# Performance work log

Hardware: AMD Instinct MI355X
Metric: run time of the kernel (lower is better)

Reference implementation:

```python
import jax, jax.numpy as jnp
import numpy as np

D_MODEL = 1024
N_HEADS = 16
HEAD_DIM = D_MODEL // N_HEADS


def setup_inputs() -> dict:
    key = jax.random.key(0)
    ks = jax.random.split(key, 12)
    B, L = 2, 2048
    s = 1.0 / np.sqrt(D_MODEL)
    inp = {
        "q": jax.random.normal(ks[0], (B, L, D_MODEL), dtype=jnp.float32),
        "k": jax.random.normal(ks[1], (B, L, D_MODEL), dtype=jnp.float32),
        "v": jax.random.normal(ks[2], (B, L, D_MODEL), dtype=jnp.float32),
        "mask": jax.random.randint(ks[3], (B, L), 0, 2).astype(jnp.bool_),
        "Wq": jax.random.normal(ks[4], (D_MODEL, D_MODEL), dtype=jnp.float32) * s,
        "bq": jnp.zeros((D_MODEL,), dtype=jnp.float32),
        "Wk": jax.random.normal(ks[5], (D_MODEL, D_MODEL), dtype=jnp.float32) * s,
        "bk": jnp.zeros((D_MODEL,), dtype=jnp.float32),
        "Wv": jax.random.normal(ks[6], (D_MODEL, D_MODEL), dtype=jnp.float32) * s,
        "bv": jnp.zeros((D_MODEL,), dtype=jnp.float32),
        "Wo": jax.random.normal(ks[7], (D_MODEL, D_MODEL), dtype=jnp.float32) * s,
        "bo": jnp.zeros((D_MODEL,), dtype=jnp.float32),
    }
    return inp


def reference(q, k, v, mask, Wq, bq, Wk, bk, Wv, bv, Wo, bo):
    B, Lq, _ = q.shape
    Lk = k.shape[1]
    # torch Linear: y = x @ W.T + b; W is [out, in]
    Q = (jnp.einsum("bld,ed->ble", q, Wq) + bq).reshape(B, Lq, N_HEADS, HEAD_DIM).transpose(0, 2, 1, 3)
    K = (jnp.einsum("bld,ed->ble", k, Wk) + bk).reshape(B, Lk, N_HEADS, HEAD_DIM).transpose(0, 2, 1, 3)
    V = (jnp.einsum("bld,ed->ble", v, Wv) + bv).reshape(B, Lk, N_HEADS, HEAD_DIM).transpose(0, 2, 1, 3)
    scale = 1.0 / np.sqrt(HEAD_DIM).astype(np.float32)
    scores = jnp.einsum("bhqd,bhkd->bhqk", Q, K) * scale  # [B,H,Lq,Lk]
    # mask: True = masked out; broadcast (B,1,1,Lk)
    scores = jnp.where(mask[:, None, None, :], -jnp.inf, scores)
    attn = jax.nn.softmax(scores, axis=-1)
    out = jnp.einsum("bhqk,bhkd->bhqd", attn, V)  # [B,H,Lq,hd]
    out = out.transpose(0, 2, 1, 3).reshape(B, Lq, D_MODEL)
    return jnp.einsum("bld,ed->ble", out, Wo) + bo
```

## Files before the change

kernel.cpp:

```cpp
#include <hip/hip_runtime.h>

typedef unsigned short u16;
typedef __bf16 bf16x8 __attribute__((ext_vector_type(8)));
typedef float f32x4 __attribute__((ext_vector_type(4)));
typedef unsigned int u32x4 __attribute__((ext_vector_type(4)));
typedef unsigned int u32x2 __attribute__((ext_vector_type(2)));

#define MFMA16(a, b, c) __builtin_amdgcn_mfma_f32_16x16x32_bf16((a), (b), (c), 0, 0, 0)

__device__ __forceinline__ u16 f2bf(float f) {
    unsigned u = __builtin_bit_cast(unsigned, f);
    u = u + 0x7FFFu + ((u >> 16) & 1u);
    return (u16)(u >> 16);
}
__device__ __forceinline__ unsigned pk2(float a, float b) {
    return (unsigned)f2bf(a) | ((unsigned)f2bf(b) << 16);
}
__device__ __forceinline__ u32x4 pk8(f32x4 a, f32x4 b) {
    u32x4 r;
    r[0] = pk2(a[0], a[1]); r[1] = pk2(a[2], a[3]);
    r[2] = pk2(b[0], b[1]); r[3] = pk2(b[2], b[3]);
    return r;
}
__device__ __forceinline__ unsigned cvtpk(float a, float b) {
    unsigned r;
    asm("v_cvt_pk_bf16_f32 %0, %1, %2" : "=v"(r) : "v"(a), "v"(b));
    return r;
}
__device__ __forceinline__ float exp2_fast(float x) {
    float r;
    asm("v_exp_f32 %0, %1" : "=v"(r) : "v"(x));
    return r;
}
__device__ __forceinline__ void lds_load16(const u16* g, u16* l) {
    __builtin_amdgcn_global_load_lds(
        (const __attribute__((address_space(1))) void*)g,
        (__attribute__((address_space(3))) void*)l, 16, 0, 0);
}

#define QSCALE 0.18033688011112042f
#define FIXMAX 13.0f

__global__ __launch_bounds__(256) void convert_bf16(
    const float* __restrict__ q, const float* __restrict__ k, const float* __restrict__ v,
    const float* __restrict__ Wq, const float* __restrict__ Wk, const float* __restrict__ Wv,
    const float* __restrict__ Wo, u16* __restrict__ dst)
{
    const size_t i = ((size_t)blockIdx.x * 256 + threadIdx.x) * 8;
    const size_t QE = 4194304, WE = 1048576;
    const float* s;
    if (i < QE) s = q + i;
    else if (i < 2 * QE) s = k + (i - QE);
    else if (i < 3 * QE) s = v + (i - 2 * QE);
    else {
        size_t j = i - 3 * QE;
        if (j < WE) s = Wq + j;
        else if (j < 2 * WE) s = Wk + (j - WE);
        else if (j < 3 * WE) s = Wv + (j - 2 * WE);
        else s = Wo + (j - 3 * WE);
    }
    f32x4 a = *(const f32x4*)s;
    f32x4 b = *(const f32x4*)(s + 4);
    *(u32x4*)(dst + i) = pk8(a, b);
}

template <bool SW>
__device__ __forceinline__ void gemm128_core(
    const u16* __restrict__ A, const u16* __restrict__ B,
    int m0, int n0, u16* As, u16* Bs, int tid, f32x4 acc[4][4])
{
    const int wv = tid >> 6, lane = tid & 63, quad = lane >> 4, l16 = lane & 15;
    const int mh = (wv >> 1) * 64, nh = (wv & 1) * 64;
    const int segA0 = wv * 128 + lane;
    const int segA1 = wv * 128 + 64 + lane;
    const int ra0 = segA0 >> 2, ca0 = (segA0 & 3) * 8;
    const int ra1 = segA1 >> 2, ca1 = (segA1 & 3) * 8;
    u16* ldsA0 = &As[(wv * 128) * 8];
    u16* ldsA1 = &As[(wv * 128 + 64) * 8];
    u16* ldsB0 = &Bs[(wv * 128) * 8];
    u16* ldsB1 = &Bs[(wv * 128 + 64) * 8];
    const u16* gA = A + (size_t)m0 * 1024;
    const u16* gB = B + (size_t)n0 * 1024;

    for (int t = 0; t < 32; t++) {
        const int k0 = t * 32;
        __syncthreads();
        lds_load16(gA + (size_t)ra0 * 1024 + k0 + ca0, ldsA0);
        lds_load16(gA + (size_t)ra1 * 1024 + k0 + ca1, ldsA1);
        lds_load16(gB + (size_t)ra0 * 1024 + k0 + ca0, ldsB0);
        lds_load16(gB + (size_t)ra1 * 1024 + k0 + ca1, ldsB1);
        __syncthreads();
        bf16x8 af[4], bfr[4];
        #pragma unroll
        for (int mi = 0; mi < 4; mi++)
            af[mi] = *(const bf16x8*)&As[(mh + mi * 16 + l16) * 32 + quad * 8];
        #pragma unroll
        for (int ni = 0; ni < 4; ni++)
            bfr[ni] = *(const bf16x8*)&Bs[(nh + ni * 16 + l16) * 32 + quad * 8];
        #pragma unroll
        for (int mi = 0; mi < 4; mi++)
            #pragma unroll
            for (int ni = 0; ni < 4; ni++)
                acc[mi][ni] = SW ? MFMA16(bfr[ni], af[mi], acc[mi][ni])
                                 : MFMA16(af[mi], bfr[ni], acc[mi][ni]);
    }
}

__global__ __launch_bounds__(256) void qkv_bf(
    const u16* __restrict__ qb, const u16* __restrict__ kb, const u16* __restrict__ vb,
    const u16* __restrict__ wq, const u16* __restrict__ wk, const u16* __restrict__ wvv,
    const float* __restrict__ bq, const float* __restrict__ bk, const float* __restrict__ bv,
    u16* __restrict__ Qh, u16* __restrict__ Kh, u16* __restrict__ Vt)
{
    __shared__ alignas(16) u16 As[128 * 32];
    __shared__ alignas(16) u16 Bs[128 * 32];
    const int z = blockIdx.z;
    const u16* A = (z == 0) ? qb : (z == 1) ? kb : vb;
    const u16* B = (z == 0) ? wq : (z == 1) ? wk : wvv;
    const float* bias = (z == 0) ? bq : (z == 1) ? bk : bv;
    const int tid = threadIdx.x;
    const int id = blockIdx.x + (blockIdx.y << 3);
    const int xd = id >> 5;
    const int yd = ((id & 7) << 2) | ((id >> 3) & 3);
    const int m0 = yd * 128, n0 = xd * 128;
    const int wv = tid >> 6, lane = tid & 63, quad = lane >> 4, l16 = lane & 15;
    const int mh = (wv >> 1) * 64, nh = (wv & 1) * 64;

    f32x4 acc[4][4];
    #pragma unroll
    for (int i = 0; i < 4; i++)
        #pragma unroll
        for (int j = 0; j < 4; j++) acc[i][j] = (f32x4){0.f, 0.f, 0.f, 0.f};

    if (z == 2) gemm128_core<true>(A, B, m0, n0, As, Bs, tid, acc);
    else        gemm128_core<false>(A, B, m0, n0, As, Bs, tid, acc);

    if (z < 2) {
        const float scl = (z == 0) ? QSCALE : 1.0f;
        u16* outp = (z == 0) ? Qh : Kh;
        #pragma unroll
        for (int ni = 0; ni < 4; ni++) {
            const int n = n0 + nh + ni * 16 + l16;
            const float bval = bias[n];
            const int h = n >> 6, d = n & 63;
            #pragma unroll
            for (int mi = 0; mi < 4; mi++) {
                const int mbase = m0 + mh + mi * 16 + quad * 4;
                #pragma unroll
                for (int r = 0; r < 4; r++) {
                    const int m = mbase + r;
                    const int bb = m >> 11, l = m & 2047;
                    const float val = (acc[mi][ni][r] + bval) * scl;
                    outp[(((size_t)(bb * 16 + h) * 2048 + l) << 6) + d] = f2bf(val);
                }
            }
        }
    } else {
        const int mW = m0 + mh;
        const int bb = mW >> 11;
        const int l0 = mW & 2047;
        #pragma unroll
        for (int ni = 0; ni < 4; ni++) {
            const int nb = n0 + nh + ni * 16 + quad * 4;
            const f32x4 bv4 = *(const f32x4*)&bias[nb];
            const int h = nb >> 6, d0 = nb & 63;
            u16* vrow = Vt + ((size_t)(bb * 16 + h) * 64 + d0) * 2048;
            #pragma unroll
            for (int mi = 0; mi < 4; mi++) {
                const int l = l0 + mi * 16 + l16;
                #pragma unroll
                for (int r = 0; r < 4; r++)
                    vrow[(size_t)r * 2048 + l] = f2bf(acc[mi][ni][r] + bv4[r]);
            }
        }
    }
}

__global__ __launch_bounds__(256) void out_bf(
    const u16* __restrict__ Ob, const u16* __restrict__ wo,
    const float* __restrict__ bo, float* __restrict__ out)
{
    __shared__ alignas(16) u16 As[128 * 32];
    __shared__ alignas(16) u16 Bs[128 * 32];
    const int tid = threadIdx.x;
    const int id = blockIdx.x + (blockIdx.y << 3);
    const int xd = id >> 5;
    const int yd = ((id & 7) << 2) | ((id >> 3) & 3);
    const int m0 = yd * 128, n0 = xd * 128;
    const int wv = tid >> 6, lane = tid & 63, quad = lane >> 4, l16 = lane & 15;
    const int mh = (wv >> 1) * 64, nh = (wv & 1) * 64;

    f32x4 acc[4][4];
    #pragma unroll
    for (int i = 0; i < 4; i++)
        #pragma unroll
        for (int j = 0; j < 4; j++) acc[i][j] = (f32x4){0.f, 0.f, 0.f, 0.f};

    gemm128_core<false>(Ob, wo, m0, n0, As, Bs, tid, acc);

    #pragma unroll
    for (int ni = 0; ni < 4; ni++) {
        const int n = n0 + nh + ni * 16 + l16;
        const float bval = bo[n];
        #pragma unroll
        for (int mi = 0; mi < 4; mi++) {
            const int mbase = m0 + mh + mi * 16 + quad * 4;
            #pragma unroll
            for (int r = 0; r < 4; r++)
                out[(size_t)(mbase + r) * 1024 + n] = acc[mi][ni][r] + bval;
        }
    }
}

__global__ __launch_bounds__(256) void attn10(
    const u16* __restrict__ Qh, const u16* __restrict__ Kh,
    const u16* __restrict__ Vt, const int* __restrict__ mask,
    u16* __restrict__ Ob)
{
    __shared__ alignas(16) u16 Ks[2][64 * 64];
    __shared__ alignas(16) u16 Vs[2][64 * 64];
    __shared__ alignas(16) float Ms[2][64];

    const int tid = threadIdx.x;
    const int blk = blockIdx.x;
    const int bh = blk & 31, qt = blk >> 5;
    const int b = bh >> 4, h = bh & 15;
    const int wv = tid >> 6, lane = tid & 63, quad = lane >> 4, l16 = lane & 15;

    const int qbase = qt * 128 + wv * 32;
    const u16* Qb = Qh + ((size_t)bh * 2048 + qbase) * 64;
    bf16x8 qf[2][2];
    #pragma unroll
    for (int sub = 0; sub < 2; sub++)
        #pragma unroll
        for (int hf = 0; hf < 2; hf++)
            qf[sub][hf] = *(const bf16x8*)(Qb + (sub * 16 + l16) * 64 + hf * 32 + quad * 8);

    const u32x4 onebits = {0x3F803F80u, 0x3F803F80u, 0x3F803F80u, 0x3F803F80u};
    const bf16x8 onesf = __builtin_bit_cast(bf16x8, onebits);

    const u16* Kb = Kh + (size_t)bh * 2048 * 64;
    const u16* Vb = Vt + (size_t)bh * 64 * 2048;
    const int* mb = mask + b * 2048;

    const int urow = lane >> 3;
    const int cunit = (lane & 7) ^ urow;
    const int u0 = wv * 16 + urow, u1 = u0 + 8;
    const int ki0 = (u0 & 3) | (((u0 >> 4) & 1) << 2) | (((u0 >> 2) & 3) << 3) | ((u0 >> 5) << 5);
    const int ki1 = (u1 & 3) | (((u1 >> 4) & 1) << 2) | (((u1 >> 2) & 3) << 3) | ((u1 >> 5) << 5);
    const u16* gk0 = Kb + (size_t)ki0 * 64 + cunit * 8;
    const u16* gk1 = Kb + (size_t)ki1 * 64 + cunit * 8;
    const u16* gv0 = Vb + (size_t)u0 * 2048 + cunit * 8;
    const u16* gv1 = Vb + (size_t)u1 * 2048 + cunit * 8;

    lds_load16(gk0, &Ks[0][wv * 1024]);
    lds_load16(gk1, &Ks[0][wv * 1024 + 512]);
    lds_load16(gv0, &Vs[0][wv * 1024]);
    lds_load16(gv1, &Vs[0][wv * 1024 + 512]);
    float rm = (tid < 64) ? (mb[tid] ? -1e30f : -FIXMAX) : 0.f;

    f32x4 o[2][4];
    #pragma unroll
    for (int sub = 0; sub < 2; sub++)
        #pragma unroll
        for (int db = 0; db < 4; db++) o[sub][db] = (f32x4){0.f, 0.f, 0.f, 0.f};
    f32x4 accL[2];
    accL[0] = (f32x4){0.f, 0.f, 0.f, 0.f};
    accL[1] = (f32x4){0.f, 0.f, 0.f, 0.f};

    const int x0 = l16 & 7;

    for (int kc = 0; kc < 32; kc++) {
        const int bi = kc & 1;
        if (tid < 64) Ms[bi][tid] = rm;
        __syncthreads();

        if (kc < 31) {
            const int off = (kc + 1) * 64;
            const int nbi = bi ^ 1;
            lds_load16(gk0 + (size_t)off * 64, &Ks[nbi][wv * 1024]);
            lds_load16(gk1 + (size_t)off * 64, &Ks[nbi][wv * 1024 + 512]);
            lds_load16(gv0 + off, &Vs[nbi][wv * 1024]);
            lds_load16(gv1 + off, &Vs[nbi][wv * 1024 + 512]);
            rm = (tid < 64) ? (mb[off + tid] ? -1e30f : -FIXMAX) : 0.f;
        }

        const u16* KsB = Ks[bi];
        const u16* VsB = Vs[bi];

        f32x4 st[2][4];
        __builtin_amdgcn_s_setprio(1);
        #pragma unroll
        for (int nb = 0; nb < 4; nb++) {
            const f32x4 mneg = *(const f32x4*)&Ms[bi][((nb >> 1) << 5) + (quad << 3) + ((nb & 1) << 2)];
            const bf16x8 kf0 = *(const bf16x8*)&KsB[(nb * 16 + l16) * 64 + ((quad ^ x0) << 3)];
            const bf16x8 kf1 = *(const bf16x8*)&KsB[(nb * 16 + l16) * 64 + (((4 | quad) ^ x0) << 3)];
            #pragma unroll
            for (int sub = 0; sub < 2; sub++) {
                f32x4 z = mneg;
                z = MFMA16(kf0, qf[sub][0], z);
                z = MFMA16(kf1, qf[sub][1], z);
                st[sub][nb] = z;
            }
        }
        __builtin_amdgcn_s_setprio(0);

        bf16x8 pf[2][2];
        #pragma unroll
        for (int sub = 0; sub < 2; sub++) {
            #pragma unroll
            for (int nb = 0; nb < 4; nb++)
                #pragma unroll
                for (int r = 0; r < 4; r++) st[sub][nb][r] = exp2_fast(st[sub][nb][r]);
            u32x4 w0, w1;
            w0[0] = cvtpk(st[sub][0][0], st[sub][0][1]);
            w0[1] = cvtpk(st[sub][0][2], st[sub][0][3]);
            w0[2] = cvtpk(st[sub][1][0], st[sub][1][1]);
            w0[3] = cvtpk(st[sub][1][2], st[sub][1][3]);
            w1[0] = cvtpk(st[sub][2][0], st[sub][2][1]);
            w1[1] = cvtpk(st[sub][2][2], st[sub][2][3]);
            w1[2] = cvtpk(st[sub][3][0], st[sub][3][1]);
            w1[3] = cvtpk(st[sub][3][2], st[sub][3][3]);
            pf[sub][0] = __builtin_bit_cast(bf16x8, w0);
            pf[sub][1] = __builtin_bit_cast(bf16x8, w1);
        }

        __builtin_amdgcn_s_setprio(1);
        #pragma unroll
        for (int db = 0; db < 4; db++) {
            const bf16x8 vf0 = *(const bf16x8*)&VsB[(db * 16 + l16) * 64 + ((quad ^ x0) << 3)];
            const bf16x8 vf1 = *(const bf16x8*)&VsB[(db * 16 + l16) * 64 + (((4 | quad) ^ x0) << 3)];
            #pragma unroll
            for (int sub = 0; sub < 2; sub++) {
                o[sub][db] = MFMA16(pf[sub][0], vf0, o[sub][db]);
                o[sub][db] = MFMA16(pf[sub][1], vf1, o[sub][db]);
            }
        }
        #pragma unroll
        for (int sub = 0; sub < 2; sub++) {
            accL[sub] = MFMA16(pf[sub][0], onesf, accL[sub]);
            accL[sub] = MFMA16(pf[sub][1], onesf, accL[sub]);
        }
        __builtin_amdgcn_s_setprio(0);
        asm volatile("" ::: "memory");
    }

    #pragma unroll
    for (int sub = 0; sub < 2; sub++) {
        #pragma unroll
        for (int r = 0; r < 4; r++) {
            const float lr = __builtin_amdgcn_rcpf(accL[sub][r]);
            const int qrow = qt * 128 + wv * 32 + sub * 16 + quad * 4 + r;
            #pragma unroll
            for (int db = 0; db < 4; db++)
                Ob[((size_t)(b * 2048 + qrow)) * 1024 + h * 64 + db * 16 + l16] =
                    f2bf(o[sub][db][r] * lr);
        }
    }
}

__global__ __launch_bounds__(256) void qkv_gemm(
    const float* __restrict__ q, const float* __restrict__ k, const float* __restrict__ v,
    const float* __restrict__ Wq, const float* __restrict__ Wk, const float* __restrict__ Wv,
    const float* __restrict__ bq, const float* __restrict__ bk, const float* __restrict__ bv,
    u16* __restrict__ Qh, u16* __restrict__ Kh, u16* __restrict__ Vt)
{
    __shared__ alignas(16) u16 As[128 * 40];
    __shared__ alignas(16) u16 Bs[128 * 40];
    const int z = blockIdx.z;
    const float* A    = (z == 0) ? q  : (z == 1) ? k  : v;
    const float* W    = (z == 0) ? Wq : (z == 1) ? Wk : Wv;
    const float* bias = (z == 0) ? bq : (z == 1) ? bk : bv;
    const int tid = threadIdx.x;
    const int m0 = blockIdx.y * 128, n0 = blockIdx.x * 128;
    const int row = tid >> 1, cseg = tid & 1;
    const float* ga = A + (size_t)(m0 + row) * 1024 + cseg * 16;
    const float* gb = W + (size_t)(n0 + row) * 1024 + cseg * 16;
    const int wv = tid >> 6, lane = tid & 63, quad = lane >> 4, l16 = lane & 15;
    const int mh = (wv >> 1) * 64, nh = (wv & 1) * 64;

    f32x4 acc[4][4];
    for (int i = 0; i < 4; i++)
        for (int j = 0; j < 4; j++) acc[i][j] = (f32x4){0.f, 0.f, 0.f, 0.f};

    f32x4 ra[4], rb[4];
    for (int i = 0; i < 4; i++) {
        ra[i] = *(const f32x4*)(ga + i * 4);
        rb[i] = *(const f32x4*)(gb + i * 4);
    }
    for (int t = 0; t < 32; t++) {
        __syncthreads();
        *(u32x4*)&As[row * 40 + cseg * 16]     = pk8(ra[0], ra[1]);
        *(u32x4*)&As[row * 40 + cseg * 16 + 8] = pk8(ra[2], ra[3]);
        *(u32x4*)&Bs[row * 40 + cseg * 16]     = pk8(rb[0], rb[1]);
        *(u32x4*)&Bs[row * 40 + cseg * 16 + 8] = pk8(rb[2], rb[3]);
        __syncthreads();
        if (t < 31) {
            const int k0 = (t + 1) * 32;
            for (int i = 0; i < 4; i++) {
                ra[i] = *(const f32x4*)(ga + k0 + i * 4);
                rb[i] = *(const f32x4*)(gb + k0 + i * 4);
            }
        }
        bf16x8 af[4], bfr[4];
        for (int mi = 0; mi < 4; mi++)
            af[mi] = *(const bf16x8*)&As[(mh + mi * 16 + l16) * 40 + quad * 8];
        for (int ni = 0; ni < 4; ni++)
            bfr[ni] = *(const bf16x8*)&Bs[(nh + ni * 16 + l16) * 40 + quad * 8];
        for (int mi = 0; mi < 4; mi++)
            for (int ni = 0; ni < 4; ni++)
                acc[mi][ni] = MFMA16(af[mi], bfr[ni], acc[mi][ni]);
    }
    const float scl = (z == 0) ? QSCALE : 1.0f;
    u16* outp = (z == 0) ? Qh : (z == 1) ? Kh : Vt;
    for (int ni = 0; ni < 4; ni++) {
        const int n = n0 + nh + ni * 16 + l16;
        const float bval = bias[n];
        const int h = n >> 6, d = n & 63;
        for (int mi = 0; mi < 4; mi++) {
            const int mbase = m0 + mh + mi * 16 + quad * 4;
            for (int r = 0; r < 4; r++) {
                const int m = mbase + r;
                const int bb = m >> 11, l = m & 2047;
                const float val = (acc[mi][ni][r] + bval) * scl;
                size_t idx;
                if (z < 2) idx = (((size_t)(bb * 16 + h) * 2048 + l) << 6) + d;
                else       idx = (((size_t)(bb * 16 + h) * 64 + d) << 11) + l;
                outp[idx] = f2bf(val);
            }
        }
    }
}

__global__ __launch_bounds__(256) void out_gemm(
    const u16* __restrict__ Ob, const float* __restrict__ Wo,
    const float* __restrict__ bo, float* __restrict__ out)
{
    __shared__ alignas(16) u16 As[128 * 40];
    __shared__ alignas(16) u16 Bs[128 * 40];
    const int tid = threadIdx.x;
    const int m0 = blockIdx.y * 128, n0 = blockIdx.x * 128;
    const int row = tid >> 1, cseg = tid & 1;
    const u16* ga = Ob + (size_t)(m0 + row) * 1024 + cseg * 16;
    const float* gb = Wo + (size_t)(n0 + row) * 1024 + cseg * 16;
    const int wv = tid >> 6, lane = tid & 63, quad = lane >> 4, l16 = lane & 15;
    const int mh = (wv >> 1) * 64, nh = (wv & 1) * 64;

    f32x4 acc[4][4];
    for (int i = 0; i < 4; i++)
        for (int j = 0; j < 4; j++) acc[i][j] = (f32x4){0.f, 0.f, 0.f, 0.f};

    u32x4 ra0 = *(const u32x4*)(ga);
    u32x4 ra1 = *(const u32x4*)(ga + 8);
    f32x4 rb[4];
    for (int i = 0; i < 4; i++) rb[i] = *(const f32x4*)(gb + i * 4);

    for (int t = 0; t < 32; t++) {
        __syncthreads();
        *(u32x4*)&As[row * 40 + cseg * 16]     = ra0;
        *(u32x4*)&As[row * 40 + cseg * 16 + 8] = ra1;
        *(u32x4*)&Bs[row * 40 + cseg * 16]     = pk8(rb[0], rb[1]);
        *(u32x4*)&Bs[row * 40 + cseg * 16 + 8] = pk8(rb[2], rb[3]);
        __syncthreads();
        if (t < 31) {
            const int k0 = (t + 1) * 32;
            ra0 = *(const u32x4*)(ga + k0);
            ra1 = *(const u32x4*)(ga + k0 + 8);
            for (int i = 0; i < 4; i++) rb[i] = *(const f32x4*)(gb + k0 + i * 4);
        }
        bf16x8 af[4], bfr[4];
        for (int mi = 0; mi < 4; mi++)
            af[mi] = *(const bf16x8*)&As[(mh + mi * 16 + l16) * 40 + quad * 8];
        for (int ni = 0; ni < 4; ni++)
            bfr[ni] = *(const bf16x8*)&Bs[(nh + ni * 16 + l16) * 40 + quad * 8];
        for (int mi = 0; mi < 4; mi++)
            for (int ni = 0; ni < 4; ni++)
                acc[mi][ni] = MFMA16(af[mi], bfr[ni], acc[mi][ni]);
    }
    for (int ni = 0; ni < 4; ni++) {
        const int n = n0 + nh + ni * 16 + l16;
        const float bval = bo[n];
        for (int mi = 0; mi < 4; mi++) {
            const int mbase = m0 + mh + mi * 16 + quad * 4;
            for (int r = 0; r < 4; r++)
                out[(size_t)(mbase + r) * 1024 + n] = acc[mi][ni][r] + bval;
        }
    }
}

extern "C" void kernel_launch(void* const* d_in, const int* in_sizes, int n_in,
                              void* d_out, int out_size, void* d_ws, size_t ws_size,
                              hipStream_t stream)
{
    (void)in_sizes; (void)n_in; (void)out_size;
    const float* q  = (const float*)d_in[0];
    const float* k  = (const float*)d_in[1];
    const float* v  = (const float*)d_in[2];
    const int* mask = (const int*)d_in[3];
    const float* Wq = (const float*)d_in[4];
    const float* bq = (const float*)d_in[5];
    const float* Wk = (const float*)d_in[6];
    const float* bk = (const float*)d_in[7];
    const float* Wv = (const float*)d_in[8];
    const float* bv = (const float*)d_in[9];
    const float* Wo = (const float*)d_in[10];
    const float* bo = (const float*)d_in[11];
    float* out = (float*)d_out;

    u16* ws = (u16*)d_ws;
    const size_t QE = 4194304, WE = 1048576;
    const size_t NEED = (6 * QE + 4 * WE) * 2;

    if (ws_size >= NEED) {
        u16* qbf = ws;
        u16* kbf = ws + QE;
        u16* vbf = ws + 2 * QE;
        u16* wqb = ws + 3 * QE;
        u16* wkb = wqb + WE;
        u16* wvb = wqb + 2 * WE;
        u16* wob = wqb + 3 * WE;
        u16* Qh  = ws + 3 * QE + 4 * WE;
        u16* Kh  = Qh + QE;
        u16* Vth = Qh + 2 * QE;
        u16* Obp = qbf;
        convert_bf16<<<dim3(8192), 256, 0, stream>>>(q, k, v, Wq, Wk, Wv, Wo, ws);
        qkv_bf<<<dim3(8, 32, 3), 256, 0, stream>>>(qbf, kbf, vbf, wqb, wkb, wvb,
                                                   bq, bk, bv, Qh, Kh, Vth);
        attn10<<<dim3(512), 256, 0, stream>>>(Qh, Kh, Vth, mask, Obp);
        out_bf<<<dim3(8, 32), 256, 0, stream>>>(Obp, wob, bo, out);
    } else {
        u16* Qh  = ws;
        u16* Kh  = ws + QE;
        u16* Vth = ws + 2 * QE;
        u16* Obp = ws + 3 * QE;
        qkv_gemm<<<dim3(8, 32, 3), 256, 0, stream>>>(q, k, v, Wq, Wk, Wv,
                                                     bq, bk, bv, Qh, Kh, Vth);
        attn10<<<dim3(512), 256, 0, stream>>>(Qh, Kh, Vth, mask, Obp);
        out_gemm<<<dim3(8, 32), 256, 0, stream>>>(Obp, Wo, bo, out);
    }
}
```

Before: 226.8 us.

## Double-buffer LDS tiles in GEMM core with XOR-swizzled layout

The shared 128x128 GEMM core used by the QKV and output projections now double-buffers its A and B tiles in LDS. It prefetches the next K-slice while computing the current one, which cuts the barriers per iteration from two to one. The LDS layout also gets an XOR swizzle on the 16-byte column chunks, applied on both the direct-to-LDS write and the fragment read, to reduce bank conflicts. The cost is twice the LDS per block, which may lower occupancy.

```diff
diff --git a/kernel.cpp b/kernel.cpp
--- a/kernel.cpp
+++ b/kernel.cpp
@@ -71,32 +71,39 @@
 {
     const int wv = tid >> 6, lane = tid & 63, quad = lane >> 4, l16 = lane & 15;
     const int mh = (wv >> 1) * 64, nh = (wv & 1) * 64;
-    const int segA0 = wv * 128 + lane;
-    const int segA1 = wv * 128 + 64 + lane;
-    const int ra0 = segA0 >> 2, ca0 = (segA0 & 3) * 8;
-    const int ra1 = segA1 >> 2, ca1 = (segA1 & 3) * 8;
-    u16* ldsA0 = &As[(wv * 128) * 8];
-    u16* ldsA1 = &As[(wv * 128 + 64) * 8];
-    u16* ldsB0 = &Bs[(wv * 128) * 8];
-    u16* ldsB1 = &Bs[(wv * 128 + 64) * 8];
-    const u16* gA = A + (size_t)m0 * 1024;
-    const u16* gB = B + (size_t)n0 * 1024;
+    const int cunit = (lane & 3) ^ ((lane >> 3) & 3);
+    const int r0 = wv * 32 + (lane >> 2);
+    const u16* gA = A + (size_t)(m0 + r0) * 1024 + cunit * 8;
+    const u16* gB = B + (size_t)(n0 + r0) * 1024 + cunit * 8;
+    const int xsw = (l16 >> 1) & 3;
+
+    lds_load16(gA, &As[wv * 1024]);
+    lds_load16(gA + 16 * 1024, &As[wv * 1024 + 512]);
+    lds_load16(gB, &Bs[wv * 1024]);
+    lds_load16(gB + 16 * 1024, &Bs[wv * 1024 + 512]);
 
     for (int t = 0; t < 32; t++) {
-        const int k0 = t * 32;
+        const int bi = t & 1;
         __syncthreads();
-        lds_load16(gA + (size_t)ra0 * 1024 + k0 + ca0, ldsA0);
-        lds_load16(gA + (size_t)ra1 * 1024 + k0 + ca1, ldsA1);
-        lds_load16(gB + (size_t)ra0 * 1024 + k0 + ca0, ldsB0);
-        lds_load16(gB + (size_t)ra1 * 1024 + k0 + ca1, ldsB1);
-        __syncthreads();
+
+        if (t < 31) {
+            const int k0 = (t + 1) * 32;
+            const int nb = bi ^ 1;
+            lds_load16(gA + k0, &As[nb * 4096 + wv * 1024]);
+            lds_load16(gA + 16 * 1024 + k0, &As[nb * 4096 + wv * 1024 + 512]);
+            lds_load16(gB + k0, &Bs[nb * 4096 + wv * 1024]);
+            lds_load16(gB + 16 * 1024 + k0, &Bs[nb * 4096 + wv * 1024 + 512]);
+        }
+
+        const u16* Ab = &As[bi * 4096];
+        const u16* Bb = &Bs[bi * 4096];
         bf16x8 af[4], bfr[4];
         #pragma unroll
         for (int mi = 0; mi < 4; mi++)
-            af[mi] = *(const bf16x8*)&As[(mh + mi * 16 + l16) * 32 + quad * 8];
+            af[mi] = *(const bf16x8*)&Ab[(mh + mi * 16 + l16) * 32 + ((quad ^ xsw) << 3)];
         #pragma unroll
         for (int ni = 0; ni < 4; ni++)
-            bfr[ni] = *(const bf16x8*)&Bs[(nh + ni * 16 + l16) * 32 + quad * 8];
+            bfr[ni] = *(const bf16x8*)&Bb[(nh + ni * 16 + l16) * 32 + ((quad ^ xsw) << 3)];
         #pragma unroll
         for (int mi = 0; mi < 4; mi++)
             #pragma unroll
@@ -112,8 +119,8 @@
     const float* __restrict__ bq, const float* __restrict__ bk, const float* __restrict__ bv,
     u16* __restrict__ Qh, u16* __restrict__ Kh, u16* __restrict__ Vt)
 {
-    __shared__ alignas(16) u16 As[128 * 32];
-    __shared__ alignas(16) u16 Bs[128 * 32];
+    __shared__ alignas(16) u16 As[2 * 4096];
+    __shared__ alignas(16) u16 Bs[2 * 4096];
     const int z = blockIdx.z;
     const u16* A = (z == 0) ? qb : (z == 1) ? kb : vb;
     const u16* B = (z == 0) ? wq : (z == 1) ? wk : wvv;
@@ -180,8 +187,8 @@
     const u16* __restrict__ Ob, const u16* __restrict__ wo,
     const float* __restrict__ bo, float* __restrict__ out)
 {
-    __shared__ alignas(16) u16 As[128 * 32];
-    __shared__ alignas(16) u16 Bs[128 * 32];
+    __shared__ alignas(16) u16 As[2 * 4096];
+    __shared__ alignas(16) u16 Bs[2 * 4096];
     const int tid = threadIdx.x;
     const int id = blockIdx.x + (blockIdx.y << 3);
     const int xd = id >> 5;
```

Result: slower. 235.7 us (+3.9%).
